# Optimization experiments

Hardware: AMD Instinct MI355X
Metric: run time of the kernel (lower is better)

## Reference

```python
import jax, jax.numpy as jnp
import numpy as np

NEG_INF = jnp.finfo(jnp.float32).min

def setup_inputs() -> dict:
    key = jax.random.key(0)
    k1, k2, k3, k4 = jax.random.split(key, 4)
    B, H, S, DK, DV = 2, 16, 2048, 64, 64
    Q = jax.random.normal(k1, (B, H, S, DK), dtype=jnp.float32)
    K = jax.random.normal(k2, (B, H, S, DK), dtype=jnp.float32)
    V = jax.random.normal(k3, (B, H, S, DV), dtype=jnp.float32)
    mask = jax.random.randint(k4, (B, 1, S, S), 0, 2, dtype=jnp.int32)
    return {"Q": Q, "K": K, "V": V, "mask": mask}

def reference(Q, K, V, mask):
    d_k = Q.shape[-1]
    # scores: [B, H, Sq, Sk]
    scores = jnp.einsum('bhqd,bhkd->bhqk', Q, K) / jnp.sqrt(jnp.float32(d_k))
    scores = jnp.where(mask == 0, NEG_INF, scores)
    attn_weights = jax.nn.softmax(scores, axis=-1)
    # dropout p=0.0 -> identity (eval-mode reference)
    output = jnp.einsum('bhqk,bhkv->bhqv', attn_weights, V)
    return (output, attn_weights)
```

## Files before the change

kernel.cpp:

```cpp
#include <hip/hip_runtime.h>


typedef __attribute__((ext_vector_type(4))) float f32x4;
typedef __attribute__((ext_vector_type(8))) short s16x8;
typedef __attribute__((ext_vector_type(4))) unsigned short u16x4;
typedef __attribute__((ext_vector_type(8))) unsigned short u16x8;

#define S_LEN 2048
#define D_DIM 64
#define H_NUM 16
#define B_NUM 2
#define NT    32
#define SW    32
#define QSCALE 0.18033688011112042f

__device__ __forceinline__ int swz(int row, int colByte) {
  return row * 128 + (colByte ^ ((row & 7) << 4));
}

__device__ __forceinline__ unsigned short f2bf(float f) {
  unsigned int x = __builtin_bit_cast(unsigned int, f);
  x = (x + 0x7FFFu + ((x >> 16) & 1u)) >> 16;
  return (unsigned short)x;
}

__device__ __forceinline__ unsigned cvt_pk_bf16(float lo, float hi) {
  unsigned r;
  asm("v_cvt_pk_bf16_f32 %0, %1, %2" : "=v"(r) : "v"(lo), "v"(hi));
  return r;
}

__device__ __forceinline__ f32x4 mfma16(f32x4 acc, s16x8 a, s16x8 b) {
  return __builtin_amdgcn_mfma_f32_16x16x32_bf16(a, b, acc, 0, 0, 0);
}


__global__ __launch_bounds__(256) void prep_kernel(
    const float* __restrict__ Q, const float* __restrict__ K,
    const float* __restrict__ V, const int* __restrict__ m,
    u16x4* __restrict__ Q16, u16x4* __restrict__ K16,
    unsigned short* __restrict__ VT, unsigned long long* __restrict__ bits)
{
  const int blk = blockIdx.x;
  const int tid = threadIdx.x;

  if (blk < 1024) {
    __shared__ unsigned short t[64][72];
    const int bh = blk >> 5;
    const int st = blk & 31;
    const float* src = V + ((size_t)bh * S_LEN + st * 64) * D_DIM;
    const int r0 = tid >> 4;
    const int c  = (tid & 15) * 4;
#pragma unroll
    for (int i = 0; i < 4; ++i) {
      const int r = r0 + i * 16;
      float4 v = *(const float4*)(src + r * D_DIM + c);
      t[c + 0][r] = f2bf(v.x); t[c + 1][r] = f2bf(v.y);
      t[c + 2][r] = f2bf(v.z); t[c + 3][r] = f2bf(v.w);
    }
    __syncthreads();
#pragma unroll
    for (int i = 0; i < 4; ++i) {
      const int idx = tid + i * 256;
      const int d = idx >> 4;
      const int s4 = (idx & 15) * 4;
      u16x4 o = {t[d][s4], t[d][s4 + 1], t[d][s4 + 2], t[d][s4 + 3]};
      *(u16x4*)(VT + ((size_t)bh * D_DIM + d) * S_LEN + st * 64 + s4) = o;
    }
  } else if (blk < 2048) {
    const int n4 = B_NUM * H_NUM * S_LEN * D_DIM / 4;
    const int step = 1024 * 256;
    for (int i = (blk - 1024) * 256 + tid; i < n4; i += step) {
      float4 q = ((const float4*)Q)[i];
      Q16[i] = u16x4{f2bf(q.x * QSCALE), f2bf(q.y * QSCALE),
                     f2bf(q.z * QSCALE), f2bf(q.w * QSCALE)};
      float4 k = ((const float4*)K)[i];
      K16[i] = u16x4{f2bf(k.x), f2bf(k.y), f2bf(k.z), f2bf(k.w)};
    }
  } else {
    const int total = B_NUM * S_LEN * S_LEN;
    const int step  = 1024 * 256;
    for (int i = (blk - 2048) * 256 + tid; i < total; i += step) {
      unsigned long long b = __ballot(m[i] != 0);
      if ((tid & 63) == 0) bits[i >> 6] = b;
    }
  }
}


__global__ __launch_bounds__(256) void attn_fused_kernel(
    const unsigned short* __restrict__ Q16, const unsigned short* __restrict__ K16,
    const unsigned short* __restrict__ VT16, const unsigned long long* __restrict__ Mb,
    float* __restrict__ Op, float* __restrict__ Wp)
{
  const int tid  = threadIdx.x;
  const int lane = tid & 63;
  const int wv   = tid >> 6;
  const int l15  = lane & 15;
  const int g4   = lane >> 4;

  const int wg = blockIdx.x;
  const int lg = (wg & 7) * 128 + (wg >> 3);
  const int qt = lg & 31;
  const int bh = lg >> 5;
  const int b  = bh >> 4;

  __shared__ __align__(16) char lds[40960];
  char* Kbuf = lds;
  char* Vbuf = lds + 16384;
  char* Ps   = lds + 32768 + (wv << 11);

  const unsigned short* Qg16 = Q16 + ((size_t)bh * S_LEN + qt * 64 + wv * 16 + l15) * D_DIM + g4 * 8;
  const unsigned short* Kg16 = K16 + (size_t)bh * S_LEN * D_DIM;
  const unsigned short* Vg   = VT16 + (size_t)bh * D_DIM * S_LEN;
  float* Og = Op + ((size_t)bh * S_LEN + qt * 64) * D_DIM;
  float* Wg = Wp + ((size_t)bh * S_LEN + qt * 64) * S_LEN;
  const unsigned long long* Mg = Mb + ((size_t)b * S_LEN + qt * 64) * SW;

  const s16x8 qa0 = *(const s16x8*)Qg16;
  const s16x8 qa1 = *(const s16x8*)(Qg16 + 32);

  f32x4 oacc[4];
#pragma unroll
  for (int i = 0; i < 4; ++i) oacc[i] = f32x4{0.f, 0.f, 0.f, 0.f};
  float lp[4] = {0.f, 0.f, 0.f, 0.f};

  const int qrow = wv * 16 + g4 * 4;

  const int sr  = tid >> 3;
  const int ss  = tid & 7;
  const int ssb = ss * 16;

  {
    u16x8 k0 = *(const u16x8*)(Kg16 + (size_t)sr * D_DIM + ss * 8);
    u16x8 k1 = *(const u16x8*)(Kg16 + (size_t)(sr + 32) * D_DIM + ss * 8);
    u16x8 v0 = *(const u16x8*)(Vg + (size_t)sr * S_LEN + ss * 8);
    u16x8 v1 = *(const u16x8*)(Vg + (size_t)(sr + 32) * S_LEN + ss * 8);
    *(u16x8*)(Kbuf + swz(sr, ssb))      = k0;
    *(u16x8*)(Kbuf + swz(sr + 32, ssb)) = k1;
    *(u16x8*)(Vbuf + swz(sr, ssb))      = v0;
    *(u16x8*)(Vbuf + swz(sr + 32, ssb)) = v1;
  }
  __syncthreads();

  int cur = 0;
  for (int kt = 0; kt < NT; ++kt) {
    const int ktn = (kt + 1 < NT) ? kt + 1 : kt;
    u16x8 kr0 = *(const u16x8*)(Kg16 + (size_t)(ktn * 64 + sr) * D_DIM + ss * 8);
    u16x8 kr1 = *(const u16x8*)(Kg16 + (size_t)(ktn * 64 + sr + 32) * D_DIM + ss * 8);
    u16x8 vr0 = *(const u16x8*)(Vg + (size_t)sr * S_LEN + ktn * 64 + ss * 8);
    u16x8 vr1 = *(const u16x8*)(Vg + (size_t)(sr + 32) * S_LEN + ktn * 64 + ss * 8);
    __builtin_amdgcn_sched_barrier(0);

    char* Kc = Kbuf + cur * 8192;
    char* Vc = Vbuf + cur * 8192;

    unsigned long long mw[4];
#pragma unroll
    for (int r = 0; r < 4; ++r) mw[r] = Mg[(qrow + r) * SW + kt];

    f32x4 sacc[4];
#pragma unroll
    for (int i = 0; i < 4; ++i) sacc[i] = f32x4{0.f, 0.f, 0.f, 0.f};
#pragma unroll
    for (int ct = 0; ct < 4; ++ct) {
      s16x8 b0 = *(const s16x8*)(Kc + swz(ct * 16 + l15, g4 * 16));
      s16x8 b1 = *(const s16x8*)(Kc + swz(ct * 16 + l15, g4 * 16 + 64));
      sacc[ct] = mfma16(sacc[ct], qa0, b0);
      sacc[ct] = mfma16(sacc[ct], qa1, b1);
    }

#pragma unroll
    for (int ct = 0; ct < 4; ++ct) {
      float ev[4];
#pragma unroll
      for (int r = 0; r < 4; ++r) {
        float e = __builtin_amdgcn_exp2f(sacc[ct][r]);
        e = ((mw[r] >> (ct * 16 + l15)) & 1ull) ? e : 0.f;
        lp[r] += e;
        ev[r] = e;
      }
      const unsigned w01 = cvt_pk_bf16(ev[0], ev[1]);
      const unsigned w23 = cvt_pk_bf16(ev[2], ev[3]);
      const int colb = (ct * 16 + l15) * 2;
      *(unsigned short*)(Ps + swz(g4 * 4 + 0, colb)) = (unsigned short)w01;
      *(unsigned short*)(Ps + swz(g4 * 4 + 1, colb)) = (unsigned short)(w01 >> 16);
      *(unsigned short*)(Ps + swz(g4 * 4 + 2, colb)) = (unsigned short)w23;
      *(unsigned short*)(Ps + swz(g4 * 4 + 3, colb)) = (unsigned short)(w23 >> 16);
    }
    asm volatile("s_waitcnt lgkmcnt(0)" ::: "memory");
    __builtin_amdgcn_sched_barrier(0);

    const s16x8 pa0 = *(const s16x8*)(Ps + swz(l15, g4 * 16));
    const s16x8 pa1 = *(const s16x8*)(Ps + swz(l15, g4 * 16 + 64));
#pragma unroll
    for (int ct = 0; ct < 4; ++ct) {
      s16x8 v0 = *(const s16x8*)(Vc + swz(ct * 16 + l15, g4 * 16));
      s16x8 v1 = *(const s16x8*)(Vc + swz(ct * 16 + l15, g4 * 16 + 64));
      oacc[ct] = mfma16(oacc[ct], pa0, v0);
      oacc[ct] = mfma16(oacc[ct], pa1, v1);
    }

    char* Kn = Kbuf + (cur ^ 1) * 8192;
    char* Vn = Vbuf + (cur ^ 1) * 8192;
    *(u16x8*)(Kn + swz(sr, ssb))      = kr0;
    *(u16x8*)(Kn + swz(sr + 32, ssb)) = kr1;
    *(u16x8*)(Vn + swz(sr, ssb))      = vr0;
    *(u16x8*)(Vn + swz(sr + 32, ssb)) = vr1;
    __syncthreads();
    cur ^= 1;
  }

#pragma unroll
  for (int r = 0; r < 4; ++r) {
    float v = lp[r];
    v += __shfl_xor(v, 1);
    v += __shfl_xor(v, 2);
    v += __shfl_xor(v, 4);
    v += __shfl_xor(v, 8);
    lp[r] = 1.0f / v;
  }

#pragma unroll
  for (int ct = 0; ct < 4; ++ct)
#pragma unroll
    for (int r = 0; r < 4; ++r)
      Og[(size_t)(qrow + r) * D_DIM + ct * 16 + l15] = oacc[ct][r] * lp[r];

  __builtin_amdgcn_sched_barrier(0);

  s16x8 kb0[4], kb1[4];
#pragma unroll
  for (int ct = 0; ct < 4; ++ct) {
    const unsigned short* kp = Kg16 + (size_t)(ct * 16 + l15) * D_DIM + g4 * 8;
    kb0[ct] = *(const s16x8*)kp;
    kb1[ct] = *(const s16x8*)(kp + 32);
  }

  for (int kt = 0; kt < NT; ++kt) {
    const int ktn = (kt < NT - 1) ? kt + 1 : kt;
    s16x8 nk0[4], nk1[4];
#pragma unroll
    for (int ct = 0; ct < 4; ++ct) {
      const unsigned short* kp = Kg16 + (size_t)(ktn * 64 + ct * 16 + l15) * D_DIM + g4 * 8;
      nk0[ct] = *(const s16x8*)kp;
      nk1[ct] = *(const s16x8*)(kp + 32);
    }

    unsigned long long mw[4];
#pragma unroll
    for (int r = 0; r < 4; ++r) mw[r] = Mg[(qrow + r) * SW + kt];

    f32x4 sacc[4];
#pragma unroll
    for (int i = 0; i < 4; ++i) sacc[i] = f32x4{0.f, 0.f, 0.f, 0.f};
#pragma unroll
    for (int ct = 0; ct < 4; ++ct) {
      sacc[ct] = mfma16(sacc[ct], qa0, kb0[ct]);
      sacc[ct] = mfma16(sacc[ct], qa1, kb1[ct]);
    }

#pragma unroll
    for (int ct = 0; ct < 4; ++ct) {
#pragma unroll
      for (int r = 0; r < 4; ++r) {
        float e = __builtin_amdgcn_exp2f(sacc[ct][r]);
        e = ((mw[r] >> (ct * 16 + l15)) & 1ull) ? e * lp[r] : 0.f;
        __builtin_nontemporal_store(e,
            Wg + (size_t)(qrow + r) * S_LEN + kt * 64 + ct * 16 + l15);
      }
    }
#pragma unroll
    for (int ct = 0; ct < 4; ++ct) { kb0[ct] = nk0[ct]; kb1[ct] = nk1[ct]; }
  }
}


template <int USE_BITS>
__global__ __launch_bounds__(256) void attn_fwd_kernel(
    const float* __restrict__ Qp, const float* __restrict__ Kp, const float* __restrict__ Vp,
    const unsigned long long* __restrict__ Mb, const int* __restrict__ Mi,
    float* __restrict__ Op, float* __restrict__ Wp)
{
  const int tid  = threadIdx.x;
  const int lane = tid & 63;
  const int wv   = tid >> 6;
  const int l15  = lane & 15;
  const int g4   = lane >> 4;

  const int wg = blockIdx.x;
  const int lg = (wg & 7) * 128 + (wg >> 3);
  const int qt = lg & 31;
  const int bh = lg >> 5;
  const int b  = bh >> 4;

  __shared__ __align__(16) char lds[32768];
  char* Qs  = lds;
  char* Ks  = lds + 8192;
  char* VTs = lds + 16384;
  char* Ps  = lds + 24576 + (wv << 11);

  const float* Qg = Qp + ((size_t)bh * S_LEN + qt * 64) * D_DIM;
  const float* Kg = Kp + (size_t)bh * S_LEN * D_DIM;
  const float* Vg = Vp + (size_t)bh * S_LEN * D_DIM;
  float* Og = Op + ((size_t)bh * S_LEN + qt * 64) * D_DIM;
  float* Wg = Wp + ((size_t)bh * S_LEN + qt * 64) * S_LEN;
  const unsigned long long* Mg = Mb + ((size_t)b * S_LEN + qt * 64) * SW;
  const int* Mig = Mi + ((size_t)b * S_LEN + qt * 64) * S_LEN;

  {
    const int r0 = tid >> 4;
    const int c  = (tid & 15) * 4;
#pragma unroll
    for (int i = 0; i < 4; ++i) {
      const int r = r0 + i * 16;
      float4 v = *(const float4*)(Qg + r * D_DIM + c);
      ushort4 p; p.x = f2bf(v.x); p.y = f2bf(v.y); p.z = f2bf(v.z); p.w = f2bf(v.w);
      *(ushort4*)(Qs + swz(r, c * 2)) = p;
    }
  }
  __syncthreads();
  const s16x8 qa0 = *(const s16x8*)(Qs + swz(wv * 16 + l15, g4 * 16));
  const s16x8 qa1 = *(const s16x8*)(Qs + swz(wv * 16 + l15, g4 * 16 + 64));

  f32x4 oacc[4];
#pragma unroll
  for (int i = 0; i < 4; ++i) oacc[i] = f32x4{0.f, 0.f, 0.f, 0.f};
  float lp[4] = {0.f, 0.f, 0.f, 0.f};

  const int qrow = wv * 16 + g4 * 4;

  for (int kt = 0; kt < NT; ++kt) {
    __syncthreads();
    {
      const int r0 = tid >> 4;
      const int c  = (tid & 15) * 4;
      const float* Kt = Kg + kt * 64 * D_DIM;
#pragma unroll
      for (int i = 0; i < 4; ++i) {
        const int r = r0 + i * 16;
        float4 v = *(const float4*)(Kt + r * D_DIM + c);
        ushort4 p; p.x = f2bf(v.x); p.y = f2bf(v.y); p.z = f2bf(v.z); p.w = f2bf(v.w);
        *(ushort4*)(Ks + swz(r, c * 2)) = p;
      }
      const float* Vt = Vg + kt * 64 * D_DIM;
#pragma unroll
      for (int i = 0; i < 2; ++i) {
        const int rr = (tid >> 4) * 2 + i * 32;
        float4 a  = *(const float4*)(Vt + rr * D_DIM + c);
        float4 bq = *(const float4*)(Vt + (rr + 1) * D_DIM + c);
        const float av[4] = {a.x, a.y, a.z, a.w};
        const float bv[4] = {bq.x, bq.y, bq.z, bq.w};
#pragma unroll
        for (int j = 0; j < 4; ++j) {
          unsigned pk = (unsigned)f2bf(av[j]) | ((unsigned)f2bf(bv[j]) << 16);
          *(unsigned*)(VTs + swz(c + j, rr * 2)) = pk;
        }
      }
    }
    __syncthreads();

    unsigned long long mw[4] = {0, 0, 0, 0};
    if (USE_BITS) {
#pragma unroll
      for (int r = 0; r < 4; ++r) mw[r] = Mg[(qrow + r) * SW + kt];
    }

    f32x4 sacc[4];
#pragma unroll
    for (int i = 0; i < 4; ++i) sacc[i] = f32x4{0.f, 0.f, 0.f, 0.f};
#pragma unroll
    for (int ct = 0; ct < 4; ++ct) {
      s16x8 b0 = *(const s16x8*)(Ks + swz(ct * 16 + l15, g4 * 16));
      s16x8 b1 = *(const s16x8*)(Ks + swz(ct * 16 + l15, g4 * 16 + 64));
      sacc[ct] = mfma16(sacc[ct], qa0, b0);
      sacc[ct] = mfma16(sacc[ct], qa1, b1);
    }

#pragma unroll
    for (int ct = 0; ct < 4; ++ct) {
#pragma unroll
      for (int r = 0; r < 4; ++r) {
        float e = __expf(sacc[ct][r] * 0.125f);
        bool keep;
        if (USE_BITS) keep = (mw[r] >> (ct * 16 + l15)) & 1ull;
        else          keep = Mig[(size_t)(qrow + r) * S_LEN + kt * 64 + ct * 16 + l15] != 0;
        e = keep ? e : 0.f;
        lp[r] += e;
        *(unsigned short*)(Ps + swz(g4 * 4 + r, (ct * 16 + l15) * 2)) = f2bf(e);
      }
    }
    asm volatile("s_waitcnt lgkmcnt(0)" ::: "memory");
    __builtin_amdgcn_sched_barrier(0);

    const s16x8 pa0 = *(const s16x8*)(Ps + swz(l15, g4 * 16));
    const s16x8 pa1 = *(const s16x8*)(Ps + swz(l15, g4 * 16 + 64));
#pragma unroll
    for (int ct = 0; ct < 4; ++ct) {
      s16x8 v0 = *(const s16x8*)(VTs + swz(ct * 16 + l15, g4 * 16));
      s16x8 v1 = *(const s16x8*)(VTs + swz(ct * 16 + l15, g4 * 16 + 64));
      oacc[ct] = mfma16(oacc[ct], pa0, v0);
      oacc[ct] = mfma16(oacc[ct], pa1, v1);
    }
  }

#pragma unroll
  for (int r = 0; r < 4; ++r) {
    float v = lp[r];
    v += __shfl_xor(v, 1);
    v += __shfl_xor(v, 2);
    v += __shfl_xor(v, 4);
    v += __shfl_xor(v, 8);
    lp[r] = 1.0f / v;
  }

#pragma unroll
  for (int ct = 0; ct < 4; ++ct)
#pragma unroll
    for (int r = 0; r < 4; ++r)
      Og[(size_t)(qrow + r) * D_DIM + ct * 16 + l15] = oacc[ct][r] * lp[r];

  for (int kt = 0; kt < NT; ++kt) {
    __syncthreads();
    {
      const int r0 = tid >> 4;
      const int c  = (tid & 15) * 4;
      const float* Kt = Kg + kt * 64 * D_DIM;
#pragma unroll
      for (int i = 0; i < 4; ++i) {
        const int r = r0 + i * 16;
        float4 v = *(const float4*)(Kt + r * D_DIM + c);
        ushort4 p; p.x = f2bf(v.x); p.y = f2bf(v.y); p.z = f2bf(v.z); p.w = f2bf(v.w);
        *(ushort4*)(Ks + swz(r, c * 2)) = p;
      }
    }
    __syncthreads();

    unsigned long long mw[4] = {0, 0, 0, 0};
    if (USE_BITS) {
#pragma unroll
      for (int r = 0; r < 4; ++r) mw[r] = Mg[(qrow + r) * SW + kt];
    }

    f32x4 sacc[4];
#pragma unroll
    for (int i = 0; i < 4; ++i) sacc[i] = f32x4{0.f, 0.f, 0.f, 0.f};
#pragma unroll
    for (int ct = 0; ct < 4; ++ct) {
      s16x8 b0 = *(const s16x8*)(Ks + swz(ct * 16 + l15, g4 * 16));
      s16x8 b1 = *(const s16x8*)(Ks + swz(ct * 16 + l15, g4 * 16 + 64));
      sacc[ct] = mfma16(sacc[ct], qa0, b0);
      sacc[ct] = mfma16(sacc[ct], qa1, b1);
    }

#pragma unroll
    for (int ct = 0; ct < 4; ++ct) {
#pragma unroll
      for (int r = 0; r < 4; ++r) {
        float e = __expf(sacc[ct][r] * 0.125f);
        bool keep;
        if (USE_BITS) keep = (mw[r] >> (ct * 16 + l15)) & 1ull;
        else          keep = Mig[(size_t)(qrow + r) * S_LEN + kt * 64 + ct * 16 + l15] != 0;
        e = keep ? e : 0.f;
        __builtin_nontemporal_store(e * lp[r],
            Wg + (size_t)(qrow + r) * S_LEN + kt * 64 + ct * 16 + l15);
      }
    }
  }
}

extern "C" void kernel_launch(void* const* d_in, const int* in_sizes, int n_in,
                              void* d_out, int out_size, void* d_ws, size_t ws_size,
                              hipStream_t stream) {
  (void)in_sizes; (void)n_in; (void)out_size;
  const float* Q   = (const float*)d_in[0];
  const float* K   = (const float*)d_in[1];
  const float* V   = (const float*)d_in[2];
  const int* mask  = (const int*)d_in[3];
  float* Out = (float*)d_out;
  float* W   = Out + (size_t)B_NUM * H_NUM * S_LEN * D_DIM;

  const size_t bits_bytes = (size_t)(B_NUM * S_LEN * S_LEN / 64) * 8;
  const size_t t16_bytes  = (size_t)B_NUM * H_NUM * S_LEN * D_DIM * 2;
  unsigned long long* bits = (unsigned long long*)d_ws;

  if (ws_size >= bits_bytes + 3 * t16_bytes) {
    unsigned short* Q16 = (unsigned short*)((char*)d_ws + bits_bytes);
    unsigned short* K16 = Q16 + t16_bytes / 2;
    unsigned short* VT  = K16 + t16_bytes / 2;
    prep_kernel<<<3072, 256, 0, stream>>>(Q, K, V, mask,
                                          (u16x4*)Q16, (u16x4*)K16, VT, bits);
    attn_fused_kernel<<<1024, 256, 0, stream>>>(Q16, K16, VT, bits, Out, W);
  } else if (ws_size >= bits_bytes) {
    mask_pack_dummy:
    {
      attn_fwd_kernel<0><<<1024, 256, 0, stream>>>(Q, K, V, bits, mask, Out, W);
    }
  } else {
    attn_fwd_kernel<0><<<1024, 256, 0, stream>>>(Q, K, V, bits, mask, Out, W);
  }
}
```

Baseline: 262.0 us.

## Compute transposed S tile so P stays in registers, skip LDS round-trip

The first QK^T MFMA now swaps its operands, so each lane holds scores for a single query row across key positions. The exponentials can then be packed straight into the bf16 A-operand for the PV MFMA, with no trip through LDS. To match the permuted key order this implies inside each 16-key group, the prep kernel writes V^T with its key columns permuted. This removes the per-wave P scratch in LDS, its stores, the lgkmcnt wait and the scattered 2-byte writes, and shrinks shared memory to 32KB. The fallback kernel is also simplified by dropping the template and the unused bitmask path; correctness depends on the permutation exactly matching the MFMA register layout.

Result: faster. 236.5 us (-9.7%).

```diff
diff --git a/kernel.cpp b/kernel.cpp
--- a/kernel.cpp
+++ b/kernel.cpp
@@ -5,6 +5,7 @@
 typedef __attribute__((ext_vector_type(8))) short s16x8;
 typedef __attribute__((ext_vector_type(4))) unsigned short u16x4;
 typedef __attribute__((ext_vector_type(8))) unsigned short u16x8;
+typedef __attribute__((ext_vector_type(4))) unsigned int u32x4;
 
 #define S_LEN 2048
 #define D_DIM 64
@@ -62,10 +63,11 @@
 #pragma unroll
     for (int i = 0; i < 4; ++i) {
       const int idx = tid + i * 256;
-      const int d = idx >> 4;
-      const int s4 = (idx & 15) * 4;
-      u16x4 o = {t[d][s4], t[d][s4 + 1], t[d][s4 + 2], t[d][s4 + 3]};
-      *(u16x4*)(VT + ((size_t)bh * D_DIM + d) * S_LEN + st * 64 + s4) = o;
+      const int d  = idx >> 4;
+      const int t0 = (idx & 15) * 4;
+      const int sp = ((t0 >> 5) & 1) * 32 + ((t0 & 7) >> 2) * 16 + ((t0 >> 3) & 3) * 4;
+      u16x4 o = *(const u16x4*)&t[d][sp];
+      *(u16x4*)(VT + ((size_t)bh * D_DIM + d) * S_LEN + st * 64 + t0) = o;
     }
   } else if (blk < 2048) {
     const int n4 = B_NUM * H_NUM * S_LEN * D_DIM / 4;
@@ -105,10 +107,9 @@
   const int bh = lg >> 5;
   const int b  = bh >> 4;
 
-  __shared__ __align__(16) char lds[40960];
+  __shared__ __align__(16) char lds[32768];
   char* Kbuf = lds;
   char* Vbuf = lds + 16384;
-  char* Ps   = lds + 32768 + (wv << 11);
 
   const unsigned short* Qg16 = Q16 + ((size_t)bh * S_LEN + qt * 64 + wv * 16 + l15) * D_DIM + g4 * 8;
   const unsigned short* Kg16 = K16 + (size_t)bh * S_LEN * D_DIM;
@@ -123,9 +124,7 @@
   f32x4 oacc[4];
 #pragma unroll
   for (int i = 0; i < 4; ++i) oacc[i] = f32x4{0.f, 0.f, 0.f, 0.f};
-  float lp[4] = {0.f, 0.f, 0.f, 0.f};
-
-  const int qrow = wv * 16 + g4 * 4;
+  float lps = 0.f;
 
   const int sr  = tid >> 3;
   const int ss  = tid & 7;
@@ -155,9 +154,7 @@
     char* Kc = Kbuf + cur * 8192;
     char* Vc = Vbuf + cur * 8192;
 
-    unsigned long long mw[4];
-#pragma unroll
-    for (int r = 0; r < 4; ++r) mw[r] = Mg[(qrow + r) * SW + kt];
+    const unsigned long long mw = Mg[(wv * 16 + l15) * SW + kt];
 
     f32x4 sacc[4];
 #pragma unroll
@@ -166,33 +163,28 @@
     for (int ct = 0; ct < 4; ++ct) {
       s16x8 b0 = *(const s16x8*)(Kc + swz(ct * 16 + l15, g4 * 16));
       s16x8 b1 = *(const s16x8*)(Kc + swz(ct * 16 + l15, g4 * 16 + 64));
-      sacc[ct] = mfma16(sacc[ct], qa0, b0);
-      sacc[ct] = mfma16(sacc[ct], qa1, b1);
-    }
-
-#pragma unroll
-    for (int ct = 0; ct < 4; ++ct) {
-      float ev[4];
+      sacc[ct] = mfma16(sacc[ct], b0, qa0);
+      sacc[ct] = mfma16(sacc[ct], b1, qa1);
+    }
+
+    float ev[4][4];
+#pragma unroll
+    for (int ct = 0; ct < 4; ++ct) {
 #pragma unroll
       for (int r = 0; r < 4; ++r) {
         float e = __builtin_amdgcn_exp2f(sacc[ct][r]);
-        e = ((mw[r] >> (ct * 16 + l15)) & 1ull) ? e : 0.f;
-        lp[r] += e;
-        ev[r] = e;
-      }
-      const unsigned w01 = cvt_pk_bf16(ev[0], ev[1]);
-      const unsigned w23 = cvt_pk_bf16(ev[2], ev[3]);
-      const int colb = (ct * 16 + l15) * 2;
-      *(unsigned short*)(Ps + swz(g4 * 4 + 0, colb)) = (unsigned short)w01;
-      *(unsigned short*)(Ps + swz(g4 * 4 + 1, colb)) = (unsigned short)(w01 >> 16);
-      *(unsigned short*)(Ps + swz(g4 * 4 + 2, colb)) = (unsigned short)w23;
-      *(unsigned short*)(Ps + swz(g4 * 4 + 3, colb)) = (unsigned short)(w23 >> 16);
-    }
-    asm volatile("s_waitcnt lgkmcnt(0)" ::: "memory");
-    __builtin_amdgcn_sched_barrier(0);
-
-    const s16x8 pa0 = *(const s16x8*)(Ps + swz(l15, g4 * 16));
-    const s16x8 pa1 = *(const s16x8*)(Ps + swz(l15, g4 * 16 + 64));
+        e = ((mw >> (ct * 16 + g4 * 4 + r)) & 1ull) ? e : 0.f;
+        ev[ct][r] = e;
+      }
+      lps += (ev[ct][0] + ev[ct][1]) + (ev[ct][2] + ev[ct][3]);
+    }
+    const u32x4 a0 = {cvt_pk_bf16(ev[0][0], ev[0][1]), cvt_pk_bf16(ev[0][2], ev[0][3]),
+                      cvt_pk_bf16(ev[1][0], ev[1][1]), cvt_pk_bf16(ev[1][2], ev[1][3])};
+    const u32x4 a1 = {cvt_pk_bf16(ev[2][0], ev[2][1]), cvt_pk_bf16(ev[2][2], ev[2][3]),
+                      cvt_pk_bf16(ev[3][0], ev[3][1]), cvt_pk_bf16(ev[3][2], ev[3][3])};
+    const s16x8 pa0 = __builtin_bit_cast(s16x8, a0);
+    const s16x8 pa1 = __builtin_bit_cast(s16x8, a1);
+
 #pragma unroll
     for (int ct = 0; ct < 4; ++ct) {
       s16x8 v0 = *(const s16x8*)(Vc + swz(ct * 16 + l15, g4 * 16));
@@ -209,6 +201,187 @@
     *(u16x8*)(Vn + swz(sr + 32, ssb)) = vr1;
     __syncthreads();
     cur ^= 1;
+  }
+
+  lps += __shfl_xor(lps, 16);
+  lps += __shfl_xor(lps, 32);
+  const float lpr = 1.0f / lps;
+
+  float lpn[4];
+#pragma unroll
+  for (int r = 0; r < 4; ++r) lpn[r] = __shfl(lpr, g4 * 4 + r);
+
+#pragma unroll
+  for (int ct = 0; ct < 4; ++ct)
+#pragma unroll
+    for (int r = 0; r < 4; ++r)
+      Og[(size_t)(wv * 16 + g4 * 4 + r) * D_DIM + ct * 16 + l15] = oacc[ct][r] * lpn[r];
+
+  __builtin_amdgcn_sched_barrier(0);
+
+  const int qrow = wv * 16 + g4 * 4;
+  s16x8 kb0[4], kb1[4];
+#pragma unroll
+  for (int ct = 0; ct < 4; ++ct) {
+    const unsigned short* kp = Kg16 + (size_t)(ct * 16 + l15) * D_DIM + g4 * 8;
+    kb0[ct] = *(const s16x8*)kp;
+    kb1[ct] = *(const s16x8*)(kp + 32);
+  }
+
+  for (int kt = 0; kt < NT; ++kt) {
+    const int ktn = (kt < NT - 1) ? kt + 1 : kt;
+    s16x8 nk0[4], nk1[4];
+#pragma unroll
+    for (int ct = 0; ct < 4; ++ct) {
+      const unsigned short* kp = Kg16 + (size_t)(ktn * 64 + ct * 16 + l15) * D_DIM + g4 * 8;
+      nk0[ct] = *(const s16x8*)kp;
+      nk1[ct] = *(const s16x8*)(kp + 32);
+    }
+
+    unsigned long long mw[4];
+#pragma unroll
+    for (int r = 0; r < 4; ++r) mw[r] = Mg[(qrow + r) * SW + kt];
+
+    f32x4 sacc[4];
+#pragma unroll
+    for (int i = 0; i < 4; ++i) sacc[i] = f32x4{0.f, 0.f, 0.f, 0.f};
+#pragma unroll
+    for (int ct = 0; ct < 4; ++ct) {
+      sacc[ct] = mfma16(sacc[ct], qa0, kb0[ct]);
+      sacc[ct] = mfma16(sacc[ct], qa1, kb1[ct]);
+    }
+
+#pragma unroll
+    for (int ct = 0; ct < 4; ++ct) {
+#pragma unroll
+      for (int r = 0; r < 4; ++r) {
+        float e = __builtin_amdgcn_exp2f(sacc[ct][r]);
+        e = ((mw[r] >> (ct * 16 + l15)) & 1ull) ? e * lpn[r] : 0.f;
+        __builtin_nontemporal_store(e,
+            Wg + (size_t)(qrow + r) * S_LEN + kt * 64 + ct * 16 + l15);
+      }
+    }
+#pragma unroll
+    for (int ct = 0; ct < 4; ++ct) { kb0[ct] = nk0[ct]; kb1[ct] = nk1[ct]; }
+  }
+}
+
+
+__global__ __launch_bounds__(256) void attn_fwd_kernel(
+    const float* __restrict__ Qp, const float* __restrict__ Kp, const float* __restrict__ Vp,
+    const int* __restrict__ Mi, float* __restrict__ Op, float* __restrict__ Wp)
+{
+  const int tid  = threadIdx.x;
+  const int lane = tid & 63;
+  const int wv   = tid >> 6;
+  const int l15  = lane & 15;
+  const int g4   = lane >> 4;
+
+  const int wg = blockIdx.x;
+  const int lg = (wg & 7) * 128 + (wg >> 3);
+  const int qt = lg & 31;
+  const int bh = lg >> 5;
+  const int b  = bh >> 4;
+
+  __shared__ __align__(16) char lds[32768];
+  char* Qs  = lds;
+  char* Ks  = lds + 8192;
+  char* VTs = lds + 16384;
+  char* Ps  = lds + 24576 + (wv << 11);
+
+  const float* Qg = Qp + ((size_t)bh * S_LEN + qt * 64) * D_DIM;
+  const float* Kg = Kp + (size_t)bh * S_LEN * D_DIM;
+  const float* Vg = Vp + (size_t)bh * S_LEN * D_DIM;
+  float* Og = Op + ((size_t)bh * S_LEN + qt * 64) * D_DIM;
+  float* Wg = Wp + ((size_t)bh * S_LEN + qt * 64) * S_LEN;
+  const int* Mig = Mi + ((size_t)b * S_LEN + qt * 64) * S_LEN;
+
+  {
+    const int r0 = tid >> 4;
+    const int c  = (tid & 15) * 4;
+#pragma unroll
+    for (int i = 0; i < 4; ++i) {
+      const int r = r0 + i * 16;
+      float4 v = *(const float4*)(Qg + r * D_DIM + c);
+      ushort4 p; p.x = f2bf(v.x); p.y = f2bf(v.y); p.z = f2bf(v.z); p.w = f2bf(v.w);
+      *(ushort4*)(Qs + swz(r, c * 2)) = p;
+    }
+  }
+  __syncthreads();
+  const s16x8 qa0 = *(const s16x8*)(Qs + swz(wv * 16 + l15, g4 * 16));
+  const s16x8 qa1 = *(const s16x8*)(Qs + swz(wv * 16 + l15, g4 * 16 + 64));
+
+  f32x4 oacc[4];
+#pragma unroll
+  for (int i = 0; i < 4; ++i) oacc[i] = f32x4{0.f, 0.f, 0.f, 0.f};
+  float lp[4] = {0.f, 0.f, 0.f, 0.f};
+
+  const int qrow = wv * 16 + g4 * 4;
+
+  for (int kt = 0; kt < NT; ++kt) {
+    __syncthreads();
+    {
+      const int r0 = tid >> 4;
+      const int c  = (tid & 15) * 4;
+      const float* Kt = Kg + kt * 64 * D_DIM;
+#pragma unroll
+      for (int i = 0; i < 4; ++i) {
+        const int r = r0 + i * 16;
+        float4 v = *(const float4*)(Kt + r * D_DIM + c);
+        ushort4 p; p.x = f2bf(v.x); p.y = f2bf(v.y); p.z = f2bf(v.z); p.w = f2bf(v.w);
+        *(ushort4*)(Ks + swz(r, c * 2)) = p;
+      }
+      const float* Vt = Vg + kt * 64 * D_DIM;
+#pragma unroll
+      for (int i = 0; i < 2; ++i) {
+        const int rr = (tid >> 4) * 2 + i * 32;
+        float4 a  = *(const float4*)(Vt + rr * D_DIM + c);
+        float4 bq = *(const float4*)(Vt + (rr + 1) * D_DIM + c);
+        const float av[4] = {a.x, a.y, a.z, a.w};
+        const float bv[4] = {bq.x, bq.y, bq.z, bq.w};
+#pragma unroll
+        for (int j = 0; j < 4; ++j) {
+          unsigned pk = (unsigned)f2bf(av[j]) | ((unsigned)f2bf(bv[j]) << 16);
+          *(unsigned*)(VTs + swz(c + j, rr * 2)) = pk;
+        }
+      }
+    }
+    __syncthreads();
+
+    f32x4 sacc[4];
+#pragma unroll
+    for (int i = 0; i < 4; ++i) sacc[i] = f32x4{0.f, 0.f, 0.f, 0.f};
+#pragma unroll
+    for (int ct = 0; ct < 4; ++ct) {
+      s16x8 b0 = *(const s16x8*)(Ks + swz(ct * 16 + l15, g4 * 16));
+      s16x8 b1 = *(const s16x8*)(Ks + swz(ct * 16 + l15, g4 * 16 + 64));
+      sacc[ct] = mfma16(sacc[ct], qa0, b0);
+      sacc[ct] = mfma16(sacc[ct], qa1, b1);
+    }
+
+#pragma unroll
+    for (int ct = 0; ct < 4; ++ct) {
+#pragma unroll
+      for (int r = 0; r < 4; ++r) {
+        float e = __expf(sacc[ct][r] * 0.125f);
+        bool keep = Mig[(size_t)(qrow + r) * S_LEN + kt * 64 + ct * 16 + l15] != 0;
+        e = keep ? e : 0.f;
+        lp[r] += e;
+        *(unsigned short*)(Ps + swz(g4 * 4 + r, (ct * 16 + l15) * 2)) = f2bf(e);
+      }
+    }
+    asm volatile("s_waitcnt lgkmcnt(0)" ::: "memory");
+    __builtin_amdgcn_sched_barrier(0);
+
+    const s16x8 pa0 = *(const s16x8*)(Ps + swz(l15, g4 * 16));
+    const s16x8 pa1 = *(const s16x8*)(Ps + swz(l15, g4 * 16 + 64));
+#pragma unroll
+    for (int ct = 0; ct < 4; ++ct) {
+      s16x8 v0 = *(const s16x8*)(VTs + swz(ct * 16 + l15, g4 * 16));
+      s16x8 v1 = *(const s16x8*)(VTs + swz(ct * 16 + l15, g4 * 16 + 64));
+      oacc[ct] = mfma16(oacc[ct], pa0, v0);
+      oacc[ct] = mfma16(oacc[ct], pa1, v1);
+    }
   }
 
 #pragma unroll
@@ -227,109 +400,6 @@
     for (int r = 0; r < 4; ++r)
       Og[(size_t)(qrow + r) * D_DIM + ct * 16 + l15] = oacc[ct][r] * lp[r];
 
-  __builtin_amdgcn_sched_barrier(0);
-
-  s16x8 kb0[4], kb1[4];
-#pragma unroll
-  for (int ct = 0; ct < 4; ++ct) {
-    const unsigned short* kp = Kg16 + (size_t)(ct * 16 + l15) * D_DIM + g4 * 8;
-    kb0[ct] = *(const s16x8*)kp;
-    kb1[ct] = *(const s16x8*)(kp + 32);
-  }
-
-  for (int kt = 0; kt < NT; ++kt) {
-    const int ktn = (kt < NT - 1) ? kt + 1 : kt;
-    s16x8 nk0[4], nk1[4];
-#pragma unroll
-    for (int ct = 0; ct < 4; ++ct) {
-      const unsigned short* kp = Kg16 + (size_t)(ktn * 64 + ct * 16 + l15) * D_DIM + g4 * 8;
-      nk0[ct] = *(const s16x8*)kp;
-      nk1[ct] = *(const s16x8*)(kp + 32);
-    }
-
-    unsigned long long mw[4];
-#pragma unroll
-    for (int r = 0; r < 4; ++r) mw[r] = Mg[(qrow + r) * SW + kt];
-
-    f32x4 sacc[4];
-#pragma unroll
-    for (int i = 0; i < 4; ++i) sacc[i] = f32x4{0.f, 0.f, 0.f, 0.f};
-#pragma unroll
-    for (int ct = 0; ct < 4; ++ct) {
-      sacc[ct] = mfma16(sacc[ct], qa0, kb0[ct]);
-      sacc[ct] = mfma16(sacc[ct], qa1, kb1[ct]);
-    }
-
-#pragma unroll
-    for (int ct = 0; ct < 4; ++ct) {
-#pragma unroll
-      for (int r = 0; r < 4; ++r) {
-        float e = __builtin_amdgcn_exp2f(sacc[ct][r]);
-        e = ((mw[r] >> (ct * 16 + l15)) & 1ull) ? e * lp[r] : 0.f;
-        __builtin_nontemporal_store(e,
-            Wg + (size_t)(qrow + r) * S_LEN + kt * 64 + ct * 16 + l15);
-      }
-    }
-#pragma unroll
-    for (int ct = 0; ct < 4; ++ct) { kb0[ct] = nk0[ct]; kb1[ct] = nk1[ct]; }
-  }
-}
-
-
-template <int USE_BITS>
-__global__ __launch_bounds__(256) void attn_fwd_kernel(
-    const float* __restrict__ Qp, const float* __restrict__ Kp, const float* __restrict__ Vp,
-    const unsigned long long* __restrict__ Mb, const int* __restrict__ Mi,
-    float* __restrict__ Op, float* __restrict__ Wp)
-{
-  const int tid  = threadIdx.x;
-  const int lane = tid & 63;
-  const int wv   = tid >> 6;
-  const int l15  = lane & 15;
-  const int g4   = lane >> 4;
-
-  const int wg = blockIdx.x;
-  const int lg = (wg & 7) * 128 + (wg >> 3);
-  const int qt = lg & 31;
-  const int bh = lg >> 5;
-  const int b  = bh >> 4;
-
-  __shared__ __align__(16) char lds[32768];
-  char* Qs  = lds;
-  char* Ks  = lds + 8192;
-  char* VTs = lds + 16384;
-  char* Ps  = lds + 24576 + (wv << 11);
-
-  const float* Qg = Qp + ((size_t)bh * S_LEN + qt * 64) * D_DIM;
-  const float* Kg = Kp + (size_t)bh * S_LEN * D_DIM;
-  const float* Vg = Vp + (size_t)bh * S_LEN * D_DIM;
-  float* Og = Op + ((size_t)bh * S_LEN + qt * 64) * D_DIM;
-  float* Wg = Wp + ((size_t)bh * S_LEN + qt * 64) * S_LEN;
-  const unsigned long long* Mg = Mb + ((size_t)b * S_LEN + qt * 64) * SW;
-  const int* Mig = Mi + ((size_t)b * S_LEN + qt * 64) * S_LEN;
-
-  {
-    const int r0 = tid >> 4;
-    const int c  = (tid & 15) * 4;
-#pragma unroll
-    for (int i = 0; i < 4; ++i) {
-      const int r = r0 + i * 16;
-      float4 v = *(const float4*)(Qg + r * D_DIM + c);
-      ushort4 p; p.x = f2bf(v.x); p.y = f2bf(v.y); p.z = f2bf(v.z); p.w = f2bf(v.w);
-      *(ushort4*)(Qs + swz(r, c * 2)) = p;
-    }
-  }
-  __syncthreads();
-  const s16x8 qa0 = *(const s16x8*)(Qs + swz(wv * 16 + l15, g4 * 16));
-  const s16x8 qa1 = *(const s16x8*)(Qs + swz(wv * 16 + l15, g4 * 16 + 64));
-
-  f32x4 oacc[4];
-#pragma unroll
-  for (int i = 0; i < 4; ++i) oacc[i] = f32x4{0.f, 0.f, 0.f, 0.f};
-  float lp[4] = {0.f, 0.f, 0.f, 0.f};
-
-  const int qrow = wv * 16 + g4 * 4;
-
   for (int kt = 0; kt < NT; ++kt) {
     __syncthreads();
     {
@@ -343,28 +413,8 @@
         ushort4 p; p.x = f2bf(v.x); p.y = f2bf(v.y); p.z = f2bf(v.z); p.w = f2bf(v.w);
         *(ushort4*)(Ks + swz(r, c * 2)) = p;
       }
-      const float* Vt = Vg + kt * 64 * D_DIM;
-#pragma unroll
-      for (int i = 0; i < 2; ++i) {
-        const int rr = (tid >> 4) * 2 + i * 32;
-        float4 a  = *(const float4*)(Vt + rr * D_DIM + c);
-        float4 bq = *(const float4*)(Vt + (rr + 1) * D_DIM + c);
-        const float av[4] = {a.x, a.y, a.z, a.w};
-        const float bv[4] = {bq.x, bq.y, bq.z, bq.w};
-#pragma unroll
-        for (int j = 0; j < 4; ++j) {
-          unsigned pk = (unsigned)f2bf(av[j]) | ((unsigned)f2bf(bv[j]) << 16);
-          *(unsigned*)(VTs + swz(c + j, rr * 2)) = pk;
-        }
-      }
-    }
-    __syncthreads();
-
-    unsigned long long mw[4] = {0, 0, 0, 0};
-    if (USE_BITS) {
-#pragma unroll
-      for (int r = 0; r < 4; ++r) mw[r] = Mg[(qrow + r) * SW + kt];
-    }
+    }
+    __syncthreads();
 
     f32x4 sacc[4];
 #pragma unroll
@@ -382,85 +432,7 @@
 #pragma unroll
       for (int r = 0; r < 4; ++r) {
         float e = __expf(sacc[ct][r] * 0.125f);
-        bool keep;
-        if (USE_BITS) keep = (mw[r] >> (ct * 16 + l15)) & 1ull;
-        else          keep = Mig[(size_t)(qrow + r) * S_LEN + kt * 64 + ct * 16 + l15] != 0;
-        e = keep ? e : 0.f;
-        lp[r] += e;
-        *(unsigned short*)(Ps + swz(g4 * 4 + r, (ct * 16 + l15) * 2)) = f2bf(e);
-      }
-    }
-    asm volatile("s_waitcnt lgkmcnt(0)" ::: "memory");
-    __builtin_amdgcn_sched_barrier(0);
-
-    const s16x8 pa0 = *(const s16x8*)(Ps + swz(l15, g4 * 16));
-    const s16x8 pa1 = *(const s16x8*)(Ps + swz(l15, g4 * 16 + 64));
-#pragma unroll
-    for (int ct = 0; ct < 4; ++ct) {
-      s16x8 v0 = *(const s16x8*)(VTs + swz(ct * 16 + l15, g4 * 16));
-      s16x8 v1 = *(const s16x8*)(VTs + swz(ct * 16 + l15, g4 * 16 + 64));
-      oacc[ct] = mfma16(oacc[ct], pa0, v0);
-      oacc[ct] = mfma16(oacc[ct], pa1, v1);
-    }
-  }
-
-#pragma unroll
-  for (int r = 0; r < 4; ++r) {
-    float v = lp[r];
-    v += __shfl_xor(v, 1);
-    v += __shfl_xor(v, 2);
-    v += __shfl_xor(v, 4);
-    v += __shfl_xor(v, 8);
-    lp[r] = 1.0f / v;
-  }
-
-#pragma unroll
-  for (int ct = 0; ct < 4; ++ct)
-#pragma unroll
-    for (int r = 0; r < 4; ++r)
-      Og[(size_t)(qrow + r) * D_DIM + ct * 16 + l15] = oacc[ct][r] * lp[r];
-
-  for (int kt = 0; kt < NT; ++kt) {
-    __syncthreads();
-    {
-      const int r0 = tid >> 4;
-      const int c  = (tid & 15) * 4;
-      const float* Kt = Kg + kt * 64 * D_DIM;
-#pragma unroll
-      for (int i = 0; i < 4; ++i) {
-        const int r = r0 + i * 16;
-        float4 v = *(const float4*)(Kt + r * D_DIM + c);
-        ushort4 p; p.x = f2bf(v.x); p.y = f2bf(v.y); p.z = f2bf(v.z); p.w = f2bf(v.w);
-        *(ushort4*)(Ks + swz(r, c * 2)) = p;
-      }
-    }
-    __syncthreads();
-
-    unsigned long long mw[4] = {0, 0, 0, 0};
-    if (USE_BITS) {
-#pragma unroll
-      for (int r = 0; r < 4; ++r) mw[r] = Mg[(qrow + r) * SW + kt];
-    }
-
-    f32x4 sacc[4];
-#pragma unroll
-    for (int i = 0; i < 4; ++i) sacc[i] = f32x4{0.f, 0.f, 0.f, 0.f};
-#pragma unroll
-    for (int ct = 0; ct < 4; ++ct) {
-      s16x8 b0 = *(const s16x8*)(Ks + swz(ct * 16 + l15, g4 * 16));
-      s16x8 b1 = *(const s16x8*)(Ks + swz(ct * 16 + l15, g4 * 16 + 64));
-      sacc[ct] = mfma16(sacc[ct], qa0, b0);
-      sacc[ct] = mfma16(sacc[ct], qa1, b1);
-    }
-
-#pragma unroll
-    for (int ct = 0; ct < 4; ++ct) {
-#pragma unroll
-      for (int r = 0; r < 4; ++r) {
-        float e = __expf(sacc[ct][r] * 0.125f);
-        bool keep;
-        if (USE_BITS) keep = (mw[r] >> (ct * 16 + l15)) & 1ull;
-        else          keep = Mig[(size_t)(qrow + r) * S_LEN + kt * 64 + ct * 16 + l15] != 0;
+        bool keep = Mig[(size_t)(qrow + r) * S_LEN + kt * 64 + ct * 16 + l15] != 0;
         e = keep ? e : 0.f;
         __builtin_nontemporal_store(e * lp[r],
             Wg + (size_t)(qrow + r) * S_LEN + kt * 64 + ct * 16 + l15);
@@ -491,12 +463,7 @@
     prep_kernel<<<3072, 256, 0, stream>>>(Q, K, V, mask,
                                           (u16x4*)Q16, (u16x4*)K16, VT, bits);
     attn_fused_kernel<<<1024, 256, 0, stream>>>(Q16, K16, VT, bits, Out, W);
-  } else if (ws_size >= bits_bytes) {
-    mask_pack_dummy:
-    {
-      attn_fwd_kernel<0><<<1024, 256, 0, stream>>>(Q, K, V, bits, mask, Out, W);
-    }
   } else {
-    attn_fwd_kernel<0><<<1024, 256, 0, stream>>>(Q, K, V, bits, mask, Out, W);
-  }
-}
+    attn_fwd_kernel<<<1024, 256, 0, stream>>>(Q, K, V, mask, Out, W);
+  }
+}
```
